# Performance work log

Measured on AMD Instinct MI355X. Metric: run time of the kernel, lower is better.

## Reference

```python
import jax, jax.numpy as jnp
import numpy as np

B, S, H, D = 2, 2048, 16, 64


def setup_inputs() -> dict:
    key = jax.random.key(0)
    qkv = jax.random.normal(key, (B, S, 3, H, D), dtype=jnp.float32)
    return {"qkv": qkv}


def reference(qkv):
    b, s, _, h, d = qkv.shape
    q, k, v = qkv[:, :, 0], qkv[:, :, 1], qkv[:, :, 2]  # (B,S,H,D) each
    softmax_scale = 1.5 / np.sqrt(d).astype(np.float32)
    # scores[b,h,t,s] = scale * <q_t, k_s>
    scores = softmax_scale * jnp.einsum('bthd,bshd->bhts', q, k)
    # mask[t,s] = True for s >= t (upper triangle incl diag) -> zeroed out
    mask = jnp.triu(jnp.ones((s, s), dtype=bool), 0)
    log_betas = jax.nn.log_sigmoid(scores)
    # -log(1 - beta) = softplus(logits), zeroed at masked positions
    nlnb = jnp.where(mask, 0.0, jax.nn.softplus(scores))
    # cum_weight is tril(-1): log_att[t,s] = log_betas[t,s] - sum_{j>s} nlnb[t,j]
    # i.e. reverse exclusive cumsum along last axis (same math as the matmul)
    rev_excl = jnp.cumsum(nlnb[..., ::-1], axis=-1)[..., ::-1] - nlnb
    att = jnp.where(mask, 0.0, jnp.exp(log_betas - rev_excl))  # (B,H,T,S)
    rem = 1.0 - att.sum(-1)  # (B,H,T) leftover stick mass
    out = jnp.einsum('bhts,bshd->bthd', att, v)
    out = out + jnp.transpose(rem, (0, 2, 1))[..., None] * v
    return out
```

## Files before the change

kernel.cpp:

```cpp
#include <hip/hip_runtime.h>
#include <math.h>
#include <cstddef>

#define BB 2
#define SSEQ 2048
#define HH 16
#define DD 64
#define ROW 3072
#define TT 64
#define SCH 64

#define QK_STR 72
#define VT_STR 68
#define SP_STR 76

typedef __attribute__((ext_vector_type(8))) short short8;
typedef __attribute__((ext_vector_type(4))) short short4v;
typedef __attribute__((ext_vector_type(4))) float floatx4;
typedef __attribute__((ext_vector_type(4))) unsigned int uintx4;

__device__ inline short bf16_rn(float f) {
    unsigned u = __float_as_uint(f);
    return (short)((u + 0x8000u) >> 16);
}
struct bf2 { short h, l; };
__device__ inline bf2 bf16_split(float f) {
    unsigned u = __float_as_uint(f);
    unsigned hb = (u + 0x8000u) & 0xFFFF0000u;
    bf2 r;
    r.h = (short)(hb >> 16);
    r.l = bf16_rn(f - __uint_as_float(hb));
    return r;
}

__global__ __launch_bounds__(256, 2) void sb_attn_mfma2(const float* __restrict__ qkv,
                                                        float* __restrict__ out) {
    __shared__ alignas(16) short Qhi[TT * QK_STR];
    __shared__ alignas(16) short Qlo[TT * QK_STR];
    __shared__ alignas(16) short Khi[SCH * QK_STR];
    __shared__ alignas(16) short Klo[SCH * QK_STR];
    __shared__ alignas(16) short Vt[DD * VT_STR];
    __shared__ alignas(16) unsigned int spP[TT * SP_STR];
    __shared__ int wdone[4];

    const int tid  = threadIdx.x;
    const int w    = tid >> 6;
    const int lane = tid & 63;
    const int m    = lane & 15;
    const int q    = lane >> 4;
    const int wrow = w * 16;
    const int g    = tid >> 4;
    const int li   = tid & 15;

    const int bh = blockIdx.x >> 5;
    const int h  = bh & (HH - 1);
    const int b  = bh >> 4;
    const int T0 = (blockIdx.x & 31) * TT;

    const float scale = 0.1875f;
    const float* qb = qkv + (size_t)b * SSEQ * ROW + h * DD;
    const float* kb = qb + HH * DD;
    const float* vb = qb + 2 * HH * DD;

    #pragma unroll
    for (int rr = 0; rr < 4; ++rr) {
        const int r = g * 4 + rr;
        float4 v4 = *(const float4*)&qb[(size_t)(T0 + r) * ROW + li * 4];
        bf2 sx = bf16_split(v4.x * scale);
        bf2 sy = bf16_split(v4.y * scale);
        bf2 sz = bf16_split(v4.z * scale);
        bf2 sw = bf16_split(v4.w * scale);
        short4v hv = {sx.h, sy.h, sz.h, sw.h};
        short4v lv = {sx.l, sy.l, sz.l, sw.l};
        *(short4v*)&Qhi[r * QK_STR + li * 4] = hv;
        *(short4v*)&Qlo[r * QK_STR + li * 4] = lv;
    }
    if (tid < 4) wdone[tid] = 0;

    const short ONE = (short)0x3F80;
    short8 onesf;
    #pragma unroll
    for (int j = 0; j < 8; ++j) onesf[j] = ONE;
    short8 Mfrag[2][4];
    #pragma unroll
    for (int ks = 0; ks < 2; ++ks)
        #pragma unroll
        for (int n = 0; n < 4; ++n)
            #pragma unroll
            for (int j = 0; j < 8; ++j)
                Mfrag[ks][n][j] = ((ks * 32 + q * 8 + j) > (n * 16 + m)) ? ONE : (short)0;

    floatx4 oac[4] = {{0,0,0,0},{0,0,0,0},{0,0,0,0},{0,0,0,0}};
    floatx4 ctotAcc = {0,0,0,0};
    floatx4 asumAcc = {0,0,0,0};

    short* attA = (short*)&spP[wrow * SP_STR];

    int chunk = 0;
    for (int S0 = T0; S0 >= 0; S0 -= SCH, ++chunk) {
        __syncthreads();
        if (chunk > 0 && (wdone[0] & wdone[1] & wdone[2] & wdone[3])) break;

        #pragma unroll
        for (int rr = 0; rr < 4; ++rr) {
            const int r = g * 4 + rr;
            float4 v4 = *(const float4*)&kb[(size_t)(S0 + r) * ROW + li * 4];
            bf2 sx = bf16_split(v4.x);
            bf2 sy = bf16_split(v4.y);
            bf2 sz = bf16_split(v4.z);
            bf2 sw = bf16_split(v4.w);
            short4v hv = {sx.h, sy.h, sz.h, sw.h};
            short4v lv = {sx.l, sy.l, sz.l, sw.l};
            *(short4v*)&Khi[r * QK_STR + li * 4] = hv;
            *(short4v*)&Klo[r * QK_STR + li * 4] = lv;
        }
        #pragma unroll
        for (int u = 0; u < 4; ++u) {
            const int s0v = w * 16 + u * 4;
            float a0 = vb[(size_t)(S0 + s0v + 0) * ROW + lane];
            float a1 = vb[(size_t)(S0 + s0v + 1) * ROW + lane];
            float a2 = vb[(size_t)(S0 + s0v + 2) * ROW + lane];
            float a3 = vb[(size_t)(S0 + s0v + 3) * ROW + lane];
            short4v hv = {bf16_rn(a0), bf16_rn(a1), bf16_rn(a2), bf16_rn(a3)};
            *(short4v*)&Vt[lane * VT_STR + s0v] = hv;
        }
        __syncthreads();

        floatx4 acc[4] = {{0,0,0,0},{0,0,0,0},{0,0,0,0},{0,0,0,0}};
        #pragma unroll
        for (int ks = 0; ks < 2; ++ks) {
            const int ko = ks * 32 + q * 8;
            short8 Ah = *(const short8*)&Qhi[(wrow + m) * QK_STR + ko];
            short8 Al = *(const short8*)&Qlo[(wrow + m) * QK_STR + ko];
            #pragma unroll
            for (int n = 0; n < 4; ++n) {
                short8 Bh = *(const short8*)&Khi[(n * 16 + m) * QK_STR + ko];
                short8 Bl = *(const short8*)&Klo[(n * 16 + m) * QK_STR + ko];
                acc[n] = __builtin_amdgcn_mfma_f32_16x16x32_bf16(Ah, Bh, acc[n], 0, 0, 0);
                acc[n] = __builtin_amdgcn_mfma_f32_16x16x32_bf16(Ah, Bl, acc[n], 0, 0, 0);
                acc[n] = __builtin_amdgcn_mfma_f32_16x16x32_bf16(Al, Bh, acc[n], 0, 0, 0);
            }
        }

        float spv[4][4];
        #pragma unroll
        for (int n = 0; n < 4; ++n) {
            #pragma unroll
            for (int reg = 0; reg < 4; ++reg) {
                const int row = wrow + q * 4 + reg;
                const bool valid = (S0 + n * 16 + m) < (T0 + row);
                const float x = acc[n][reg];
                const float s = valid ? __logf(1.f + __expf(x)) : 0.f;
                spv[n][reg] = s;
                bf2 sl = bf16_split(s);
                spP[row * SP_STR + n * 16 + m] =
                    ((unsigned)(unsigned short)sl.h << 16) | (unsigned)(unsigned short)sl.l;
            }
        }

        short8 SAh[2], SAl[2];
        #pragma unroll
        for (int ks = 0; ks < 2; ++ks) {
            const unsigned int* pp = &spP[(wrow + m) * SP_STR + ks * 32 + q * 8];
            uintx4 r0 = *(const uintx4*)pp;
            uintx4 r1 = *(const uintx4*)(pp + 4);
            unsigned pv[8] = {r0.x, r0.y, r0.z, r0.w, r1.x, r1.y, r1.z, r1.w};
            #pragma unroll
            for (int j = 0; j < 8; ++j) {
                SAh[ks][j] = (short)(pv[j] >> 16);
                SAl[ks][j] = (short)(pv[j] & 0xFFFFu);
            }
        }

        const float Cold[4] = {ctotAcc[0], ctotAcc[1], ctotAcc[2], ctotAcc[3]};

        floatx4 rev[4] = {{0,0,0,0},{0,0,0,0},{0,0,0,0},{0,0,0,0}};
        #pragma unroll
        for (int ks = 0; ks < 2; ++ks) {
            #pragma unroll
            for (int n = 0; n < 4; ++n) {
                rev[n] = __builtin_amdgcn_mfma_f32_16x16x32_bf16(SAh[ks], Mfrag[ks][n], rev[n], 0, 0, 0);
                rev[n] = __builtin_amdgcn_mfma_f32_16x16x32_bf16(SAl[ks], Mfrag[ks][n], rev[n], 0, 0, 0);
            }
            ctotAcc = __builtin_amdgcn_mfma_f32_16x16x32_bf16(SAh[ks], onesf, ctotAcc, 0, 0, 0);
            ctotAcc = __builtin_amdgcn_mfma_f32_16x16x32_bf16(SAl[ks], onesf, ctotAcc, 0, 0, 0);
        }

        #pragma unroll
        for (int n = 0; n < 4; ++n) {
            #pragma unroll
            for (int reg = 0; reg < 4; ++reg) {
                const int row = q * 4 + reg;
                const bool valid = (S0 + n * 16 + m) < (T0 + wrow + row);
                const float y = acc[n][reg] - spv[n][reg] - rev[n][reg] - Cold[reg];
                const float a = valid ? __expf(y) : 0.f;
                attA[row * 72 + n * 16 + m] = bf16_rn(a);
            }
        }

        #pragma unroll
        for (int ks = 0; ks < 2; ++ks) {
            const int ko = ks * 32 + q * 8;
            short8 Ap = *(const short8*)&attA[m * 72 + ko];
            asumAcc = __builtin_amdgcn_mfma_f32_16x16x32_bf16(Ap, onesf, asumAcc, 0, 0, 0);
            #pragma unroll
            for (int n = 0; n < 4; ++n) {
                const short* vp = &Vt[(n * 16 + m) * VT_STR + ko];
                short4v b0 = *(const short4v*)vp;
                short4v b1 = *(const short4v*)(vp + 4);
                short8 Bv = {b0.x, b0.y, b0.z, b0.w, b1.x, b1.y, b1.z, b1.w};
                oac[n] = __builtin_amdgcn_mfma_f32_16x16x32_bf16(Ap, Bv, oac[n], 0, 0, 0);
            }
        }

        const bool myd = (ctotAcc[0] > 30.f) && (ctotAcc[1] > 30.f) &&
                         (ctotAcc[2] > 30.f) && (ctotAcc[3] > 30.f);
        const int wd = __all((int)myd);
        if (lane == 0) wdone[w] = wd;
    }

    #pragma unroll
    for (int n = 0; n < 4; ++n) {
        #pragma unroll
        for (int reg = 0; reg < 4; ++reg) {
            const int tl = wrow + q * 4 + reg;
            const int tG = T0 + tl;
            const int dc = n * 16 + m;
            const float rem = 1.f - asumAcc[reg];
            const float vt = vb[(size_t)tG * ROW + dc];
            out[(((size_t)b * SSEQ + tG) * HH + h) * DD + dc] = fmaf(rem, vt, oac[n][reg]);
        }
    }
}

extern "C" void kernel_launch(void* const* d_in, const int* in_sizes, int n_in,
                              void* d_out, int out_size, void* d_ws, size_t ws_size,
                              hipStream_t stream) {
    const float* qkv = (const float*)d_in[0];
    float* out = (float*)d_out;
    const int blocks = BB * HH * (SSEQ / TT);
    sb_attn_mfma2<<<blocks, 256, 0, stream>>>(qkv, out);
}
```

Baseline: 100.1 us.

## Replace split-bf16 MFMA emulation with single-pass fp16 MFMA

Drops the hi/lo bf16 split trick, which needed three QK MFMAs and two cumsum MFMAs per tile, and uses plain fp16 MFMA instead. Q fragments are now kept in registers rather than shared memory, and shared memory shrinks enough to allow launch_bounds of 4 blocks per CU. This cuts MFMA count, LDS traffic and conversion ALU work. The cost is accuracy: the fp16 QK logits and fp16 softplus cumsum lose precision relative to the emulated fp32 path.

```diff
diff --git a/kernel.cpp b/kernel.cpp
--- a/kernel.cpp
+++ b/kernel.cpp
@@ -9,38 +9,17 @@
 #define ROW 3072
 #define TT 64
 #define SCH 64
+#define LSTR 72
 
-#define QK_STR 72
-#define VT_STR 68
-#define SP_STR 76
+typedef __attribute__((ext_vector_type(8))) _Float16 half8;
+typedef __attribute__((ext_vector_type(4))) _Float16 half4;
+typedef __attribute__((ext_vector_type(4))) float floatx4;
 
-typedef __attribute__((ext_vector_type(8))) short short8;
-typedef __attribute__((ext_vector_type(4))) short short4v;
-typedef __attribute__((ext_vector_type(4))) float floatx4;
-typedef __attribute__((ext_vector_type(4))) unsigned int uintx4;
-
-__device__ inline short bf16_rn(float f) {
-    unsigned u = __float_as_uint(f);
-    return (short)((u + 0x8000u) >> 16);
-}
-struct bf2 { short h, l; };
-__device__ inline bf2 bf16_split(float f) {
-    unsigned u = __float_as_uint(f);
-    unsigned hb = (u + 0x8000u) & 0xFFFF0000u;
-    bf2 r;
-    r.h = (short)(hb >> 16);
-    r.l = bf16_rn(f - __uint_as_float(hb));
-    return r;
-}
-
-__global__ __launch_bounds__(256, 2) void sb_attn_mfma2(const float* __restrict__ qkv,
-                                                        float* __restrict__ out) {
-    __shared__ alignas(16) short Qhi[TT * QK_STR];
-    __shared__ alignas(16) short Qlo[TT * QK_STR];
-    __shared__ alignas(16) short Khi[SCH * QK_STR];
-    __shared__ alignas(16) short Klo[SCH * QK_STR];
-    __shared__ alignas(16) short Vt[DD * VT_STR];
-    __shared__ alignas(16) unsigned int spP[TT * SP_STR];
+__global__ __launch_bounds__(256, 4) void sb_attn_f16(const float* __restrict__ qkv,
+                                                      float* __restrict__ out) {
+    __shared__ alignas(16) _Float16 Kf[SCH * LSTR];
+    __shared__ alignas(16) _Float16 Vt[DD * LSTR];
+    __shared__ alignas(16) _Float16 spf[TT * LSTR];
     __shared__ int wdone[4];
 
     const int tid  = threadIdx.x;
@@ -62,39 +41,39 @@
     const float* kb = qb + HH * DD;
     const float* vb = qb + 2 * HH * DD;
 
+    half8 Aq[2];
     #pragma unroll
-    for (int rr = 0; rr < 4; ++rr) {
-        const int r = g * 4 + rr;
-        float4 v4 = *(const float4*)&qb[(size_t)(T0 + r) * ROW + li * 4];
-        bf2 sx = bf16_split(v4.x * scale);
-        bf2 sy = bf16_split(v4.y * scale);
-        bf2 sz = bf16_split(v4.z * scale);
-        bf2 sw = bf16_split(v4.w * scale);
-        short4v hv = {sx.h, sy.h, sz.h, sw.h};
-        short4v lv = {sx.l, sy.l, sz.l, sw.l};
-        *(short4v*)&Qhi[r * QK_STR + li * 4] = hv;
-        *(short4v*)&Qlo[r * QK_STR + li * 4] = lv;
+    for (int ks = 0; ks < 2; ++ks) {
+        const float* qp = &qb[(size_t)(T0 + wrow + m) * ROW + ks * 32 + q * 8];
+        float4 a = *(const float4*)qp;
+        float4 c = *(const float4*)(qp + 4);
+        half8 v;
+        v[0] = (_Float16)(a.x * scale); v[1] = (_Float16)(a.y * scale);
+        v[2] = (_Float16)(a.z * scale); v[3] = (_Float16)(a.w * scale);
+        v[4] = (_Float16)(c.x * scale); v[5] = (_Float16)(c.y * scale);
+        v[6] = (_Float16)(c.z * scale); v[7] = (_Float16)(c.w * scale);
+        Aq[ks] = v;
     }
     if (tid < 4) wdone[tid] = 0;
 
-    const short ONE = (short)0x3F80;
-    short8 onesf;
+    const _Float16 ONEH = (_Float16)1.0f;
+    half8 onesf;
     #pragma unroll
-    for (int j = 0; j < 8; ++j) onesf[j] = ONE;
-    short8 Mfrag[2][4];
+    for (int j = 0; j < 8; ++j) onesf[j] = ONEH;
+    half8 Mfrag[2][4];
     #pragma unroll
     for (int ks = 0; ks < 2; ++ks)
         #pragma unroll
         for (int n = 0; n < 4; ++n)
             #pragma unroll
             for (int j = 0; j < 8; ++j)
-                Mfrag[ks][n][j] = ((ks * 32 + q * 8 + j) > (n * 16 + m)) ? ONE : (short)0;
+                Mfrag[ks][n][j] = ((ks * 32 + q * 8 + j) > (n * 16 + m)) ? ONEH : (_Float16)0.0f;
 
     floatx4 oac[4] = {{0,0,0,0},{0,0,0,0},{0,0,0,0},{0,0,0,0}};
     floatx4 ctotAcc = {0,0,0,0};
     floatx4 asumAcc = {0,0,0,0};
 
-    short* attA = (short*)&spP[wrow * SP_STR];
+    _Float16* attA = &spf[wrow * LSTR];
 
     int chunk = 0;
     for (int S0 = T0; S0 >= 0; S0 -= SCH, ++chunk) {
@@ -105,14 +84,8 @@
         for (int rr = 0; rr < 4; ++rr) {
             const int r = g * 4 + rr;
             float4 v4 = *(const float4*)&kb[(size_t)(S0 + r) * ROW + li * 4];
-            bf2 sx = bf16_split(v4.x);
-            bf2 sy = bf16_split(v4.y);
-            bf2 sz = bf16_split(v4.z);
-            bf2 sw = bf16_split(v4.w);
-            short4v hv = {sx.h, sy.h, sz.h, sw.h};
-            short4v lv = {sx.l, sy.l, sz.l, sw.l};
-            *(short4v*)&Khi[r * QK_STR + li * 4] = hv;
-            *(short4v*)&Klo[r * QK_STR + li * 4] = lv;
+            half4 hv = {(_Float16)v4.x, (_Float16)v4.y, (_Float16)v4.z, (_Float16)v4.w};
+            *(half4*)&Kf[r * LSTR + li * 4] = hv;
         }
         #pragma unroll
         for (int u = 0; u < 4; ++u) {
@@ -121,8 +94,8 @@
             float a1 = vb[(size_t)(S0 + s0v + 1) * ROW + lane];
             float a2 = vb[(size_t)(S0 + s0v + 2) * ROW + lane];
             float a3 = vb[(size_t)(S0 + s0v + 3) * ROW + lane];
-            short4v hv = {bf16_rn(a0), bf16_rn(a1), bf16_rn(a2), bf16_rn(a3)};
-            *(short4v*)&Vt[lane * VT_STR + s0v] = hv;
+            half4 hv = {(_Float16)a0, (_Float16)a1, (_Float16)a2, (_Float16)a3};
+            *(half4*)&Vt[lane * LSTR + s0v] = hv;
         }
         __syncthreads();
 
@@ -130,15 +103,10 @@
         #pragma unroll
         for (int ks = 0; ks < 2; ++ks) {
             const int ko = ks * 32 + q * 8;
-            short8 Ah = *(const short8*)&Qhi[(wrow + m) * QK_STR + ko];
-            short8 Al = *(const short8*)&Qlo[(wrow + m) * QK_STR + ko];
             #pragma unroll
             for (int n = 0; n < 4; ++n) {
-                short8 Bh = *(const short8*)&Khi[(n * 16 + m) * QK_STR + ko];
-                short8 Bl = *(const short8*)&Klo[(n * 16 + m) * QK_STR + ko];
-                acc[n] = __builtin_amdgcn_mfma_f32_16x16x32_bf16(Ah, Bh, acc[n], 0, 0, 0);
-                acc[n] = __builtin_amdgcn_mfma_f32_16x16x32_bf16(Ah, Bl, acc[n], 0, 0, 0);
-                acc[n] = __builtin_amdgcn_mfma_f32_16x16x32_bf16(Al, Bh, acc[n], 0, 0, 0);
+                half8 Bv = *(const half8*)&Kf[(n * 16 + m) * LSTR + ko];
+                acc[n] = __builtin_amdgcn_mfma_f32_16x16x32_f16(Aq[ks], Bv, acc[n], 0, 0, 0);
             }
         }
 
@@ -149,28 +117,16 @@
             for (int reg = 0; reg < 4; ++reg) {
                 const int row = wrow + q * 4 + reg;
                 const bool valid = (S0 + n * 16 + m) < (T0 + row);
-                const float x = acc[n][reg];
-                const float s = valid ? __logf(1.f + __expf(x)) : 0.f;
+                const float s = valid ? __logf(1.f + __expf(acc[n][reg])) : 0.f;
                 spv[n][reg] = s;
-                bf2 sl = bf16_split(s);
-                spP[row * SP_STR + n * 16 + m] =
-                    ((unsigned)(unsigned short)sl.h << 16) | (unsigned)(unsigned short)sl.l;
+                spf[row * LSTR + n * 16 + m] = (_Float16)s;
             }
         }
 
-        short8 SAh[2], SAl[2];
+        half8 SA[2];
         #pragma unroll
-        for (int ks = 0; ks < 2; ++ks) {
-            const unsigned int* pp = &spP[(wrow + m) * SP_STR + ks * 32 + q * 8];
-            uintx4 r0 = *(const uintx4*)pp;
-            uintx4 r1 = *(const uintx4*)(pp + 4);
-            unsigned pv[8] = {r0.x, r0.y, r0.z, r0.w, r1.x, r1.y, r1.z, r1.w};
-            #pragma unroll
-            for (int j = 0; j < 8; ++j) {
-                SAh[ks][j] = (short)(pv[j] >> 16);
-                SAl[ks][j] = (short)(pv[j] & 0xFFFFu);
-            }
-        }
+        for (int ks = 0; ks < 2; ++ks)
+            SA[ks] = *(const half8*)&spf[(wrow + m) * LSTR + ks * 32 + q * 8];
 
         const float Cold[4] = {ctotAcc[0], ctotAcc[1], ctotAcc[2], ctotAcc[3]};
 
@@ -178,12 +134,9 @@
         #pragma unroll
         for (int ks = 0; ks < 2; ++ks) {
             #pragma unroll
-            for (int n = 0; n < 4; ++n) {
-                rev[n] = __builtin_amdgcn_mfma_f32_16x16x32_bf16(SAh[ks], Mfrag[ks][n], rev[n], 0, 0, 0);
-                rev[n] = __builtin_amdgcn_mfma_f32_16x16x32_bf16(SAl[ks], Mfrag[ks][n], rev[n], 0, 0, 0);
-            }
-            ctotAcc = __builtin_amdgcn_mfma_f32_16x16x32_bf16(SAh[ks], onesf, ctotAcc, 0, 0, 0);
-            ctotAcc = __builtin_amdgcn_mfma_f32_16x16x32_bf16(SAl[ks], onesf, ctotAcc, 0, 0, 0);
+            for (int n = 0; n < 4; ++n)
+                rev[n] = __builtin_amdgcn_mfma_f32_16x16x32_f16(SA[ks], Mfrag[ks][n], rev[n], 0, 0, 0);
+            ctotAcc = __builtin_amdgcn_mfma_f32_16x16x32_f16(SA[ks], onesf, ctotAcc, 0, 0, 0);
         }
 
         #pragma unroll
@@ -193,23 +146,19 @@
                 const int row = q * 4 + reg;
                 const bool valid = (S0 + n * 16 + m) < (T0 + wrow + row);
                 const float y = acc[n][reg] - spv[n][reg] - rev[n][reg] - Cold[reg];
-                const float a = valid ? __expf(y) : 0.f;
-                attA[row * 72 + n * 16 + m] = bf16_rn(a);
+                attA[row * LSTR + n * 16 + m] = valid ? (_Float16)__expf(y) : (_Float16)0.0f;
             }
         }
 
         #pragma unroll
         for (int ks = 0; ks < 2; ++ks) {
             const int ko = ks * 32 + q * 8;
-            short8 Ap = *(const short8*)&attA[m * 72 + ko];
-            asumAcc = __builtin_amdgcn_mfma_f32_16x16x32_bf16(Ap, onesf, asumAcc, 0, 0, 0);
+            half8 Ap = *(const half8*)&attA[m * LSTR + ko];
+            asumAcc = __builtin_amdgcn_mfma_f32_16x16x32_f16(Ap, onesf, asumAcc, 0, 0, 0);
             #pragma unroll
             for (int n = 0; n < 4; ++n) {
-                const short* vp = &Vt[(n * 16 + m) * VT_STR + ko];
-                short4v b0 = *(const short4v*)vp;
-                short4v b1 = *(const short4v*)(vp + 4);
-                short8 Bv = {b0.x, b0.y, b0.z, b0.w, b1.x, b1.y, b1.z, b1.w};
-                oac[n] = __builtin_amdgcn_mfma_f32_16x16x32_bf16(Ap, Bv, oac[n], 0, 0, 0);
+                half8 Bv = *(const half8*)&Vt[(n * 16 + m) * LSTR + ko];
+                oac[n] = __builtin_amdgcn_mfma_f32_16x16x32_f16(Ap, Bv, oac[n], 0, 0, 0);
             }
         }
 
@@ -239,5 +188,5 @@
     const float* qkv = (const float*)d_in[0];
     float* out = (float*)d_out;
     const int blocks = BB * HH * (SSEQ / TT);
-    sb_attn_mfma2<<<blocks, 256, 0, stream>>>(qkv, out);
+    sb_attn_f16<<<blocks, 256, 0, stream>>>(qkv, out);
 }
```

Result: slower. 102.5 us (+2.4%).
